# Optimization experiments

Measured on AMD Instinct MI355X. Metric: run time of the kernel, lower is better.

## Reference

```python
import jax, jax.numpy as jnp
import numpy as np

N_NODES = 100000
N_EDGES = 300000
D_NODE_IN = 128
D_EDGE_IN = 4
LATENT = 256
HIDDEN = 256
STEPS = 6
D_OUT = 128
LN_EPS = 1e-5


def _mlp(x, w1, b1, w2, b2):
    # hk.nets.MLP([HIDDEN, out], activation=swish): act on hidden, none on output
    return jax.nn.swish(x @ w1 + b1) @ w2 + b2


def _ln(x, scale, offset):
    m = jnp.mean(x, axis=-1, keepdims=True)
    c = x - m
    v = jnp.mean(c * c, axis=-1, keepdims=True)
    return c * jax.lax.rsqrt(v + LN_EPS) * scale + offset


def setup_inputs():
    key = jax.random.key(0)
    ks = iter(jax.random.split(key, 40))

    def w(shape):
        fan_in = shape[-2]
        return (jax.random.normal(next(ks), shape, jnp.float32) / np.sqrt(fan_in).astype(np.float32))

    inp = {}
    inp['node_features'] = jax.random.normal(next(ks), (N_NODES, D_NODE_IN), jnp.float32)
    inp['edge_features'] = jax.random.normal(next(ks), (N_EDGES, D_EDGE_IN), jnp.float32)
    inp['senders'] = jax.random.randint(next(ks), (N_EDGES,), 0, N_NODES, jnp.int32)
    inp['receivers'] = jax.random.randint(next(ks), (N_EDGES,), 0, N_NODES, jnp.int32)
    # encoder (embed) MLPs + LayerNorm
    inp['enc_node_w1'] = w((D_NODE_IN, HIDDEN)); inp['enc_node_b1'] = jnp.zeros((HIDDEN,), jnp.float32)
    inp['enc_node_w2'] = w((HIDDEN, LATENT)); inp['enc_node_b2'] = jnp.zeros((LATENT,), jnp.float32)
    inp['enc_node_ln_s'] = jnp.ones((LATENT,), jnp.float32); inp['enc_node_ln_o'] = jnp.zeros((LATENT,), jnp.float32)
    inp['enc_edge_w1'] = w((D_EDGE_IN, HIDDEN)); inp['enc_edge_b1'] = jnp.zeros((HIDDEN,), jnp.float32)
    inp['enc_edge_w2'] = w((HIDDEN, LATENT)); inp['enc_edge_b2'] = jnp.zeros((LATENT,), jnp.float32)
    inp['enc_edge_ln_s'] = jnp.ones((LATENT,), jnp.float32); inp['enc_edge_ln_o'] = jnp.zeros((LATENT,), jnp.float32)
    # processor: STEPS unshared InteractionNetwork layers, weights stacked on axis 0
    inp['pe_w1'] = w((STEPS, 3 * LATENT, HIDDEN)); inp['pe_b1'] = jnp.zeros((STEPS, HIDDEN), jnp.float32)
    inp['pe_w2'] = w((STEPS, HIDDEN, LATENT)); inp['pe_b2'] = jnp.zeros((STEPS, LATENT), jnp.float32)
    inp['pe_ln_s'] = jnp.ones((STEPS, LATENT), jnp.float32); inp['pe_ln_o'] = jnp.zeros((STEPS, LATENT), jnp.float32)
    inp['pn_w1'] = w((STEPS, 2 * LATENT, HIDDEN)); inp['pn_b1'] = jnp.zeros((STEPS, HIDDEN), jnp.float32)
    inp['pn_w2'] = w((STEPS, HIDDEN, LATENT)); inp['pn_b2'] = jnp.zeros((STEPS, LATENT), jnp.float32)
    inp['pn_ln_s'] = jnp.ones((STEPS, LATENT), jnp.float32); inp['pn_ln_o'] = jnp.zeros((STEPS, LATENT), jnp.float32)
    # decoder (output) MLP, no LayerNorm
    inp['dec_w1'] = w((LATENT, HIDDEN)); inp['dec_b1'] = jnp.zeros((HIDDEN,), jnp.float32)
    inp['dec_w2'] = w((HIDDEN, D_OUT)); inp['dec_b2'] = jnp.zeros((D_OUT,), jnp.float32)
    return inp


def reference(node_features, edge_features, senders, receivers,
              enc_node_w1, enc_node_b1, enc_node_w2, enc_node_b2, enc_node_ln_s, enc_node_ln_o,
              enc_edge_w1, enc_edge_b1, enc_edge_w2, enc_edge_b2, enc_edge_ln_s, enc_edge_ln_o,
              pe_w1, pe_b1, pe_w2, pe_b2, pe_ln_s, pe_ln_o,
              pn_w1, pn_b1, pn_w2, pn_b2, pn_ln_s, pn_ln_o,
              dec_w1, dec_b1, dec_w2, dec_b2):
    # Embed nodes and edges into latent space (MLP + LayerNorm).
    node = _ln(_mlp(node_features, enc_node_w1, enc_node_b1, enc_node_w2, enc_node_b2), enc_node_ln_s, enc_node_ln_o)
    edge = _ln(_mlp(edge_features, enc_edge_w1, enc_edge_b1, enc_edge_w2, enc_edge_b2), enc_edge_ln_s, enc_edge_ln_o)

    n_nodes = node.shape[0]

    def step(carry, p):
        node, edge = carry
        ew1, eb1, ew2, eb2, els, elo, nw1, nb1, nw2, nb2, nls, nlo = p
        # edge update: MLP(concat[edge, sender_node, receiver_node]) + residual
        msg_in = jnp.concatenate([edge, node[senders], node[receivers]], axis=-1)  # [E, 3*LATENT]
        edge = edge + _ln(_mlp(msg_in, ew1, eb1, ew2, eb2), els, elo)
        # aggregate messages to receiver nodes
        agg = jax.ops.segment_sum(edge, receivers, num_segments=n_nodes)  # [N, LATENT]
        # node update: MLP(concat[node, agg]) + residual
        node = node + _ln(_mlp(jnp.concatenate([node, agg], axis=-1), nw1, nb1, nw2, nb2), nls, nlo)
        return (node, edge), None

    (node, edge), _ = jax.lax.scan(
        step, (node, edge),
        (pe_w1, pe_b1, pe_w2, pe_b2, pe_ln_s, pe_ln_o,
         pn_w1, pn_b1, pn_w2, pn_b2, pn_ln_s, pn_ln_o))

    # decoder: plain MLP (no LayerNorm) on nodes only (node_output_size given).
    return _mlp(node, dec_w1, dec_b1, dec_w2, dec_b2)  # [N, D_OUT]
```

## Files before the change

kernel.cpp:

```cpp
#include <hip/hip_runtime.h>
#include <hip/hip_bf16.h>


#define NN 100000
#define NE 300000

typedef __attribute__((ext_vector_type(8))) short bf16x8;
typedef __attribute__((ext_vector_type(8))) unsigned short u16x8;
typedef __attribute__((ext_vector_type(4))) float f32x4;

typedef const __attribute__((address_space(1))) void cg1_t;
typedef __attribute__((address_space(3))) void l3_t;
static __device__ __forceinline__ void gld_lds16(const void* g, void* l) {
  __builtin_amdgcn_global_load_lds((cg1_t*)g, (l3_t*)l, 16, 0, 0);
}

static __device__ __forceinline__ unsigned short f2bf(float f) {
  union { float f; unsigned u; } v; v.f = f;
  unsigned r = v.u + 0x7FFFu + ((v.u >> 16) & 1u);
  return (unsigned short)(r >> 16);
}
static __device__ __forceinline__ float bf2f(unsigned short h) {
  union { unsigned u; float f; } v; v.u = ((unsigned)h) << 16;
  return v.f;
}
static __device__ __forceinline__ float swish(float x) {
  return x * __builtin_amdgcn_rcpf(1.f + __expf(-x));
}

struct KArgs {
  const float* Xf;
  unsigned short* nodeB;
  unsigned short* edgeB;
  const unsigned short* aggB;
  const int* snd;
  const int* rcv;
  const unsigned short* W1p;
  const unsigned short* W2p;
  const float* b1;
  const float* b2;
  const float* lns;
  const float* lno;
  float* outF;
  int M;
};

__global__ void pack_w(const float* __restrict__ src,
                       unsigned short* __restrict__ dst,
                       int Ksrc, int Kpad, int N) {
  src += (size_t)blockIdx.y * Ksrc * N;
  dst += (size_t)blockIdx.y * Kpad * N;
  int fi = blockIdx.x;
  int nfr = N >> 4;
  int nb = fi % nfr, kb = fi / nfr;
  int t = threadIdx.x;
  int lane = t >> 3, j = t & 7;
  int k = kb * 32 + ((lane >> 4) * 8) + j;
  int col = nb * 16 + (lane & 15);
  unsigned short v = (k < Ksrc) ? f2bf(src[(size_t)k * N + col]) : (unsigned short)0;
  dst[(size_t)fi * 512 + t] = v;
}

__global__ void zero_ws(uint4* __restrict__ p, int n16) {
  uint4 z = {0u, 0u, 0u, 0u};
  for (int i = blockIdx.x * blockDim.x + threadIdx.x; i < n16;
       i += gridDim.x * blockDim.x)
    p[i] = z;
}

__global__ void hist_k(const int* __restrict__ rcv, int* __restrict__ cnt) {
  int e = blockIdx.x * blockDim.x + threadIdx.x;
  if (e < NE) {
    int r = rcv[e]; r = r < 0 ? 0 : (r > NN - 1 ? NN - 1 : r);
    atomicAdd(&cnt[r], 1);
  }
}

__global__ __launch_bounds__(1024)
void scan_k(const int* __restrict__ cnt, int* __restrict__ off) {
  __shared__ int wsum[16];
  __shared__ int carry_s, tot_s;
  int t = threadIdx.x, lane = t & 63, w = t >> 6;
  if (t == 0) carry_s = 0;
  __syncthreads();
  for (int base = 0; base < NN; base += 1024) {
    int i = base + t;
    int v = (i < NN) ? cnt[i] : 0;
    int incl = v;
    #pragma unroll
    for (int d = 1; d < 64; d <<= 1) {
      int u = __shfl_up(incl, d);
      if (lane >= d) incl += u;
    }
    if (lane == 63) wsum[w] = incl;
    int c0 = carry_s;
    __syncthreads();
    if (t < 16) {
      int s = wsum[t];
      int isc = s;
      #pragma unroll
      for (int d = 1; d < 16; d <<= 1) {
        int u = __shfl_up(isc, d);
        if (t >= d) isc += u;
      }
      wsum[t] = isc - s;
    }
    __syncthreads();
    int excl = c0 + wsum[w] + incl - v;
    if (i < NN) off[i] = excl;
    if (t == 1023) tot_s = wsum[15] + incl;
    __syncthreads();
    if (t == 0) carry_s += tot_s;
    __syncthreads();
  }
  if (t == 0) off[NN] = carry_s;
}

__global__ void fill_k(const int* __restrict__ rcv, const int* __restrict__ off,
                       int* __restrict__ cnt2, int* __restrict__ eidx) {
  int e = blockIdx.x * blockDim.x + threadIdx.x;
  if (e < NE) {
    int r = rcv[e]; r = r < 0 ? 0 : (r > NN - 1 ? NN - 1 : r);
    int p = off[r] + atomicAdd(&cnt2[r], 1);
    if (p >= 0 && p < NE) eidx[p] = e;
  }
}

__global__ __launch_bounds__(256)
void agg_k(const unsigned short* __restrict__ edge, const int* __restrict__ off,
           const int* __restrict__ eidx, unsigned short* __restrict__ agg) {
  int t = threadIdx.x;
  int n0 = blockIdx.x * 8;
  #pragma unroll 1
  for (int u = 0; u < 8; ++u) {
    int n = n0 + u;
    if (n >= NN) return;
    int s = off[n], e = off[n + 1];
    if (s < 0) s = 0;
    if (e > NE) e = NE;
    float acc = 0.f;
    for (int i = s; i < e; ++i) {
      int eid = eidx[i];
      eid = eid < 0 ? 0 : (eid > NE - 1 ? NE - 1 : eid);
      acc += bf2f(edge[(size_t)eid * 256 + t]);
    }
    agg[(size_t)n * 256 + t] = f2bf(acc);
  }
}

template<int PHASE>
__global__ __launch_bounds__(512)
void gnn_kernel(KArgs A) {
  constexpr int K1  = PHASE==0?128 : PHASE==1?64 : PHASE==2?768 : PHASE==3?512 : 256;
  constexpr int NS1 = K1 / 64;
  constexpr int N2  = (PHASE==4) ? 128 : 256;
  constexpr int NF2 = N2 / 128;

  __shared__ __align__(16) char smem[38912];
  auto Ht  = (unsigned short (*)[264])(smem);
  float* ps    = (float*)(smem + 33792);
  float* ps2   = (float*)(smem + 35840);
  float* rs_mu = (float*)(smem + 37888);
  float* rs_rs = (float*)(smem + 38144);
  int*   lidx  = (int*)(smem + 38400);

  const int tid  = threadIdx.x;
  const int wid  = tid >> 6;
  const int lane = tid & 63;
  const int r0   = blockIdx.x * 64;
  const int M    = A.M;

  if constexpr (PHASE == 2) {
    if (tid < 64) {
      int e = r0 + tid; if (e > M - 1) e = M - 1;
      int v = A.snd[e]; v = v < 0 ? 0 : (v > NN - 1 ? NN - 1 : v);
      lidx[tid] = v;
    } else if (tid < 128) {
      int e = r0 + tid - 64; if (e > M - 1) e = M - 1;
      int v = A.rcv[e]; v = v < 0 ? 0 : (v > NN - 1 ? NN - 1 : v);
      lidx[tid] = v;
    }
  }
  __syncthreads();

  const int mrow  = lane & 15;
  const int rbase = (lane >> 4) * 4;
  const int swz   = mrow & 7;

  f32x4 zero4 = {0.f, 0.f, 0.f, 0.f};
  f32x4 acc1[4][2];
  #pragma unroll
  for (int m = 0; m < 4; ++m) { acc1[m][0] = zero4; acc1[m][1] = zero4; }

  if constexpr (PHASE <= 1) {
    auto stage = [&](int ks, int b) {
      int r = tid >> 3;
      int c = (tid & 7) ^ (r & 7);
      int row = r0 + r; if (row > M - 1) row = M - 1;
      u16x8 w;
      if constexpr (PHASE == 0) {
        const float* s = A.Xf + (size_t)row * 128 + ks * 64 + c * 8;
        float4 f0 = *(const float4*)s;
        float4 f1 = *(const float4*)(s + 4);
        w[0]=f2bf(f0.x); w[1]=f2bf(f0.y); w[2]=f2bf(f0.z); w[3]=f2bf(f0.w);
        w[4]=f2bf(f1.x); w[5]=f2bf(f1.y); w[6]=f2bf(f1.z); w[7]=f2bf(f1.w);
      } else {
        w = (u16x8){0,0,0,0,0,0,0,0};
        if (c == 0) {
          float4 f = *(const float4*)(A.Xf + (size_t)row * 4);
          w[0]=f2bf(f.x); w[1]=f2bf(f.y); w[2]=f2bf(f.z); w[3]=f2bf(f.w);
        }
      }
      *(u16x8*)(smem + b * 8192 + (tid >> 3) * 128 + (tid & 7) * 16) = w;
    };
    stage(0, 0);
    __syncthreads();
    #pragma unroll
    for (int ks = 0; ks < NS1; ++ks) {
      if (ks + 1 < NS1) stage(ks + 1, (ks + 1) & 1);
      const char* buf = smem + (ks & 1) * 8192;
      #pragma unroll
      for (int kk = 0; kk < 2; ++kk) {
        int ch = (kk * 4 + (lane >> 4)) ^ swz;
        const char* p0 = buf + mrow * 128 + ch * 16;
        bf16x8 a0 = *(const bf16x8*)(p0);
        bf16x8 a1 = *(const bf16x8*)(p0 + 16 * 128);
        bf16x8 a2 = *(const bf16x8*)(p0 + 32 * 128);
        bf16x8 a3 = *(const bf16x8*)(p0 + 48 * 128);
        const unsigned short* wb = A.W1p + ((size_t)((2 * ks + kk) * 16 + wid * 2) * 64 + lane) * 8;
        bf16x8 b0 = *(const bf16x8*)(wb);
        bf16x8 b1 = *(const bf16x8*)(wb + 512);
        acc1[0][0] = __builtin_amdgcn_mfma_f32_16x16x32_bf16(a0, b0, acc1[0][0], 0, 0, 0);
        acc1[0][1] = __builtin_amdgcn_mfma_f32_16x16x32_bf16(a0, b1, acc1[0][1], 0, 0, 0);
        acc1[1][0] = __builtin_amdgcn_mfma_f32_16x16x32_bf16(a1, b0, acc1[1][0], 0, 0, 0);
        acc1[1][1] = __builtin_amdgcn_mfma_f32_16x16x32_bf16(a1, b1, acc1[1][1], 0, 0, 0);
        acc1[2][0] = __builtin_amdgcn_mfma_f32_16x16x32_bf16(a2, b0, acc1[2][0], 0, 0, 0);
        acc1[2][1] = __builtin_amdgcn_mfma_f32_16x16x32_bf16(a2, b1, acc1[2][1], 0, 0, 0);
        acc1[3][0] = __builtin_amdgcn_mfma_f32_16x16x32_bf16(a3, b0, acc1[3][0], 0, 0, 0);
        acc1[3][1] = __builtin_amdgcn_mfma_f32_16x16x32_bf16(a3, b1, acc1[3][1], 0, 0, 0);
      }
      __syncthreads();
    }
  } else {
    int r = tid >> 3;
    int cs = ((tid & 7) ^ (r & 7)) * 8;
    int row = r0 + r; if (row > M - 1) row = M - 1;
    const unsigned short *s0 = nullptr, *s1 = nullptr, *s2 = nullptr;
    if constexpr (PHASE == 2) {
      s0 = A.edgeB + (size_t)row * 256 + cs;
      s1 = A.nodeB + (size_t)lidx[r] * 256 + cs;
      s2 = A.nodeB + (size_t)lidx[64 + r] * 256 + cs;
    } else if constexpr (PHASE == 3) {
      s0 = A.nodeB + (size_t)row * 256 + cs;
      s1 = A.aggB + (size_t)row * 256 + cs;
    } else {
      s0 = A.nodeB + (size_t)row * 256 + cs;
    }
    auto issue = [&](int ks, int b) {
      const unsigned short* src;
      if constexpr (PHASE == 2)
        src = ks < 4 ? s0 + ks * 64 : (ks < 8 ? s1 + (ks - 4) * 64 : s2 + (ks - 8) * 64);
      else if constexpr (PHASE == 3)
        src = ks < 4 ? s0 + ks * 64 : s1 + (ks - 4) * 64;
      else
        src = s0 + ks * 64;
      gld_lds16(src, smem + b * 8192 + wid * 1024);
    };
    const unsigned short* w1base = A.W1p + ((size_t)(wid * 2) * 64 + lane) * 8;
    auto load_b = [&](int ks, bf16x8* bk0, bf16x8* bk1) {
      const unsigned short* wb0 = w1base + (size_t)(2 * ks) * 16 * 512;
      const unsigned short* wb1 = w1base + (size_t)(2 * ks + 1) * 16 * 512;
      bk0[0] = *(const bf16x8*)(wb0); bk0[1] = *(const bf16x8*)(wb0 + 512);
      bk1[0] = *(const bf16x8*)(wb1); bk1[1] = *(const bf16x8*)(wb1 + 512);
    };

    issue(0, 0);
    issue(1, 1);
    bf16x8 c0[2], c1[2], n0[2], n1[2];
    load_b(0, c0, c1);
    #pragma unroll
    for (int ks = 0; ks < NS1; ++ks) {
      if (ks < NS1 - 1) asm volatile("s_waitcnt vmcnt(1)" ::: "memory");
      else              asm volatile("s_waitcnt vmcnt(0)" ::: "memory");
      __builtin_amdgcn_sched_barrier(0);
      __builtin_amdgcn_s_barrier();
      __builtin_amdgcn_sched_barrier(0);
      if (ks + 1 < NS1) load_b(ks + 1, n0, n1);
      const char* buf = smem + (ks & 1) * 8192;
      #pragma unroll
      for (int kk = 0; kk < 2; ++kk) {
        int ch = (kk * 4 + (lane >> 4)) ^ swz;
        const char* p0 = buf + mrow * 128 + ch * 16;
        bf16x8 a0 = *(const bf16x8*)(p0);
        bf16x8 a1 = *(const bf16x8*)(p0 + 16 * 128);
        bf16x8 a2 = *(const bf16x8*)(p0 + 32 * 128);
        bf16x8 a3 = *(const bf16x8*)(p0 + 48 * 128);
        bf16x8 b0 = kk ? c1[0] : c0[0];
        bf16x8 b1 = kk ? c1[1] : c0[1];
        acc1[0][0] = __builtin_amdgcn_mfma_f32_16x16x32_bf16(a0, b0, acc1[0][0], 0, 0, 0);
        acc1[0][1] = __builtin_amdgcn_mfma_f32_16x16x32_bf16(a0, b1, acc1[0][1], 0, 0, 0);
        acc1[1][0] = __builtin_amdgcn_mfma_f32_16x16x32_bf16(a1, b0, acc1[1][0], 0, 0, 0);
        acc1[1][1] = __builtin_amdgcn_mfma_f32_16x16x32_bf16(a1, b1, acc1[1][1], 0, 0, 0);
        acc1[2][0] = __builtin_amdgcn_mfma_f32_16x16x32_bf16(a2, b0, acc1[2][0], 0, 0, 0);
        acc1[2][1] = __builtin_amdgcn_mfma_f32_16x16x32_bf16(a2, b1, acc1[2][1], 0, 0, 0);
        acc1[3][0] = __builtin_amdgcn_mfma_f32_16x16x32_bf16(a3, b0, acc1[3][0], 0, 0, 0);
        acc1[3][1] = __builtin_amdgcn_mfma_f32_16x16x32_bf16(a3, b1, acc1[3][1], 0, 0, 0);
      }
      __builtin_amdgcn_sched_barrier(0);
      __builtin_amdgcn_s_barrier();
      __builtin_amdgcn_sched_barrier(0);
      if (ks + 2 < NS1) issue(ks + 2, ks & 1);
      c0[0] = n0[0]; c0[1] = n0[1]; c1[0] = n1[0]; c1[1] = n1[1];
    }
  }

  #pragma unroll
  for (int nf = 0; nf < 2; ++nf) {
    int c = wid * 32 + nf * 16 + mrow;
    float bb = A.b1[c];
    #pragma unroll
    for (int m = 0; m < 4; ++m)
      #pragma unroll
      for (int j = 0; j < 4; ++j)
        Ht[m * 16 + rbase + j][c] = f2bf(swish(acc1[m][nf][j] + bb));
  }
  __syncthreads();

  f32x4 acc2[4][NF2];
  #pragma unroll
  for (int m = 0; m < 4; ++m)
    #pragma unroll
    for (int nf = 0; nf < NF2; ++nf) acc2[m][nf] = zero4;

  const int kof = (lane >> 4) * 8;
  #pragma unroll
  for (int ks = 0; ks < 8; ++ks) {
    bf16x8 a[4], b[NF2];
    #pragma unroll
    for (int m = 0; m < 4; ++m)
      a[m] = *(const bf16x8*)&Ht[m * 16 + mrow][ks * 32 + kof];
    #pragma unroll
    for (int nf = 0; nf < NF2; ++nf)
      b[nf] = *(const bf16x8*)(A.W2p + ((size_t)(ks * (N2 / 16) + wid * NF2 + nf) * 64 + lane) * 8);
    #pragma unroll
    for (int m = 0; m < 4; ++m)
      #pragma unroll
      for (int nf = 0; nf < NF2; ++nf)
        acc2[m][nf] = __builtin_amdgcn_mfma_f32_16x16x32_bf16(a[m], b[nf], acc2[m][nf], 0, 0, 0);
  }

  if constexpr (PHASE == 4) {
    int c = wid * 16 + mrow;
    float bb = A.b2[c];
    #pragma unroll
    for (int m = 0; m < 4; ++m)
      #pragma unroll
      for (int j = 0; j < 4; ++j) {
        int rg = r0 + m * 16 + rbase + j;
        if (rg < M) A.outF[(size_t)rg * 128 + c] = acc2[m][0][j] + bb;
      }
  } else {
    const int cc0 = wid * 32 + mrow;
    const int cc1 = cc0 + 16;
    const float bb0 = A.b2[cc0];
    const float bb1 = A.b2[cc1];
    #pragma unroll
    for (int m = 0; m < 4; ++m)
      #pragma unroll
      for (int j = 0; j < 4; ++j) {
        acc2[m][0][j] += bb0;
        acc2[m][1][j] += bb1;
        float t  = acc2[m][0][j] + acc2[m][1][j];
        float t2 = acc2[m][0][j] * acc2[m][0][j] + acc2[m][1][j] * acc2[m][1][j];
        #pragma unroll
        for (int mk = 1; mk < 16; mk <<= 1) {
          t  += __shfl_xor(t, mk);
          t2 += __shfl_xor(t2, mk);
        }
        if (mrow == 0) {
          int row = m * 16 + rbase + j;
          ps [wid * 64 + row] = t;
          ps2[wid * 64 + row] = t2;
        }
      }
    __syncthreads();
    if (tid < 64) {
      float s = 0.f, q = 0.f;
      #pragma unroll
      for (int w = 0; w < 8; ++w) { s += ps[w * 64 + tid]; q += ps2[w * 64 + tid]; }
      float mu = s * (1.0f / 256.0f);
      float va = fmaxf(q * (1.0f / 256.0f) - mu * mu, 0.f);
      rs_mu[tid] = mu;
      rs_rs[tid] = __builtin_amdgcn_rsqf(va + 1e-5f);
    }
    __syncthreads();
    const float ls0 = A.lns[cc0], lo0 = A.lno[cc0];
    const float ls1 = A.lns[cc1], lo1 = A.lno[cc1];
    #pragma unroll
    for (int m = 0; m < 4; ++m)
      #pragma unroll
      for (int j = 0; j < 4; ++j) {
        int row = m * 16 + rbase + j;
        int rg = r0 + row;
        if (rg >= M) continue;
        float mu = rs_mu[row], rstd = rs_rs[row];
        float y0 = (acc2[m][0][j] - mu) * rstd * ls0 + lo0;
        float y1 = (acc2[m][1][j] - mu) * rstd * ls1 + lo1;
        size_t base = (size_t)rg * 256;
        if constexpr (PHASE == 0) {
          A.nodeB[base + cc0] = f2bf(y0);
          A.nodeB[base + cc1] = f2bf(y1);
        } else if constexpr (PHASE == 1) {
          A.edgeB[base + cc0] = f2bf(y0);
          A.edgeB[base + cc1] = f2bf(y1);
        } else if constexpr (PHASE == 2) {
          A.edgeB[base + cc0] = f2bf(bf2f(A.edgeB[base + cc0]) + y0);
          A.edgeB[base + cc1] = f2bf(bf2f(A.edgeB[base + cc1]) + y1);
        } else {
          A.nodeB[base + cc0] = f2bf(bf2f(A.nodeB[base + cc0]) + y0);
          A.nodeB[base + cc1] = f2bf(bf2f(A.nodeB[base + cc1]) + y1);
        }
      }
  }
}

extern "C" void kernel_launch(void* const* d_in, const int* in_sizes, int n_in,
                              void* d_out, int out_size, void* d_ws, size_t ws_size,
                              hipStream_t stream) {
  (void)in_sizes; (void)n_in; (void)out_size; (void)ws_size;
  const float* x_node = (const float*)d_in[0];
  const float* x_edge = (const float*)d_in[1];
  const int* snd = (const int*)d_in[2];
  const int* rcv = (const int*)d_in[3];
  const float* en_w1 = (const float*)d_in[4];
  const float* en_b1 = (const float*)d_in[5];
  const float* en_w2 = (const float*)d_in[6];
  const float* en_b2 = (const float*)d_in[7];
  const float* en_ls = (const float*)d_in[8];
  const float* en_lo = (const float*)d_in[9];
  const float* ee_w1 = (const float*)d_in[10];
  const float* ee_b1 = (const float*)d_in[11];
  const float* ee_w2 = (const float*)d_in[12];
  const float* ee_b2 = (const float*)d_in[13];
  const float* ee_ls = (const float*)d_in[14];
  const float* ee_lo = (const float*)d_in[15];
  const float* pe_w1 = (const float*)d_in[16];
  const float* pe_b1 = (const float*)d_in[17];
  const float* pe_w2 = (const float*)d_in[18];
  const float* pe_b2 = (const float*)d_in[19];
  const float* pe_ls = (const float*)d_in[20];
  const float* pe_lo = (const float*)d_in[21];
  const float* pn_w1 = (const float*)d_in[22];
  const float* pn_b1 = (const float*)d_in[23];
  const float* pn_w2 = (const float*)d_in[24];
  const float* pn_b2 = (const float*)d_in[25];
  const float* pn_ls = (const float*)d_in[26];
  const float* pn_lo = (const float*)d_in[27];
  const float* dc_w1 = (const float*)d_in[28];
  const float* dc_b1 = (const float*)d_in[29];
  const float* dc_w2 = (const float*)d_in[30];
  const float* dc_b2 = (const float*)d_in[31];

  char* ws = (char*)d_ws;
  unsigned short* edgeB = (unsigned short*)(ws);
  unsigned short* nodeB = (unsigned short*)(ws + 153600000LL);
  unsigned short* aggB  = (unsigned short*)(ws + 204800000LL);

  unsigned short* wpck = (unsigned short*)d_out;
  size_t o = 0;
  auto nxt = [&](size_t n) { unsigned short* p = wpck + o; o += n; return p; };
  unsigned short* p_en_w1 = nxt(128 * 256);
  unsigned short* p_en_w2 = nxt(256 * 256);
  unsigned short* p_ee_w1 = nxt(64 * 256);
  unsigned short* p_ee_w2 = nxt(256 * 256);
  unsigned short* p_pe_w1 = nxt((size_t)6 * 768 * 256);
  unsigned short* p_pe_w2 = nxt((size_t)6 * 256 * 256);
  unsigned short* p_pn_w1 = nxt((size_t)6 * 512 * 256);
  unsigned short* p_pn_w2 = nxt((size_t)6 * 256 * 256);
  unsigned short* p_dc_w1 = nxt(256 * 256);
  unsigned short* p_dc_w2 = nxt(256 * 128);
  const size_t DC_BYTES = (256 * 256 + 256 * 128) * 2;

  char* outc = (char*)d_out;
  int* cnt  = (int*)(outc + 6062080);
  int* cnt2 = (int*)(outc + 6462080);
  int* off  = (int*)(outc + 6862080);
  int* eidx = (int*)(outc + 7262096);

  dim3 B(512);
  pack_w<<<dim3(4 * 16, 1), B, 0, stream>>>(en_w1, p_en_w1, 128, 128, 256);
  pack_w<<<dim3(8 * 16, 1), B, 0, stream>>>(en_w2, p_en_w2, 256, 256, 256);
  pack_w<<<dim3(2 * 16, 1), B, 0, stream>>>(ee_w1, p_ee_w1, 4, 64, 256);
  pack_w<<<dim3(8 * 16, 1), B, 0, stream>>>(ee_w2, p_ee_w2, 256, 256, 256);
  pack_w<<<dim3(24 * 16, 6), B, 0, stream>>>(pe_w1, p_pe_w1, 768, 768, 256);
  pack_w<<<dim3(8 * 16, 6), B, 0, stream>>>(pe_w2, p_pe_w2, 256, 256, 256);
  pack_w<<<dim3(16 * 16, 6), B, 0, stream>>>(pn_w1, p_pn_w1, 512, 512, 256);
  pack_w<<<dim3(8 * 16, 6), B, 0, stream>>>(pn_w2, p_pn_w2, 256, 256, 256);
  pack_w<<<dim3(8 * 16, 1), B, 0, stream>>>(dc_w1, p_dc_w1, 256, 256, 256);
  pack_w<<<dim3(8 * 8, 1), B, 0, stream>>>(dc_w2, p_dc_w2, 256, 256, 128);

  zero_ws<<<dim3(196), dim3(256), 0, stream>>>((uint4*)cnt, 800000 / 16);
  hist_k<<<dim3(1172), dim3(256), 0, stream>>>(rcv, cnt);
  scan_k<<<dim3(1), dim3(1024), 0, stream>>>(cnt, off);
  fill_k<<<dim3(1172), dim3(256), 0, stream>>>(rcv, off, cnt2, eidx);

  dim3 GN(1563), GE(4688);

  {
    KArgs a{}; a.Xf = x_node; a.W1p = p_en_w1; a.W2p = p_en_w2;
    a.b1 = en_b1; a.b2 = en_b2; a.lns = en_ls; a.lno = en_lo;
    a.nodeB = nodeB; a.M = NN;
    gnn_kernel<0><<<GN, B, 0, stream>>>(a);
  }
  {
    KArgs a{}; a.Xf = x_edge; a.W1p = p_ee_w1; a.W2p = p_ee_w2;
    a.b1 = ee_b1; a.b2 = ee_b2; a.lns = ee_ls; a.lno = ee_lo;
    a.edgeB = edgeB; a.M = NE;
    gnn_kernel<1><<<GE, B, 0, stream>>>(a);
  }
  for (int s = 0; s < 6; ++s) {
    {
      KArgs a{}; a.snd = snd; a.rcv = rcv;
      a.nodeB = nodeB; a.edgeB = edgeB;
      a.W1p = p_pe_w1 + (size_t)s * 768 * 256;
      a.W2p = p_pe_w2 + (size_t)s * 256 * 256;
      a.b1 = pe_b1 + s * 256; a.b2 = pe_b2 + s * 256;
      a.lns = pe_ls + s * 256; a.lno = pe_lo + s * 256;
      a.M = NE;
      gnn_kernel<2><<<GE, B, 0, stream>>>(a);
    }
    agg_k<<<dim3(12500), dim3(256), 0, stream>>>(edgeB, off, eidx, aggB);
    {
      KArgs a{}; a.nodeB = nodeB; a.aggB = aggB;
      a.W1p = p_pn_w1 + (size_t)s * 512 * 256;
      a.W2p = p_pn_w2 + (size_t)s * 256 * 256;
      a.b1 = pn_b1 + s * 256; a.b2 = pn_b2 + s * 256;
      a.lns = pn_ls + s * 256; a.lno = pn_lo + s * 256;
      a.M = NN;
      gnn_kernel<3><<<GN, B, 0, stream>>>(a);
    }
  }
  hipMemcpyAsync((void*)aggB, p_dc_w1, DC_BYTES, hipMemcpyDeviceToDevice, stream);
  {
    KArgs a{}; a.nodeB = nodeB;
    a.W1p = (const unsigned short*)aggB;
    a.W2p = (const unsigned short*)aggB + 256 * 256;
    a.b1 = dc_b1; a.b2 = dc_b2;
    a.outF = (float*)d_out; a.M = NN;
    gnn_kernel<4><<<GN, B, 0, stream>>>(a);
  }
}
```

Measured before the change: 2.767 ms.

## Triple-buffer the A-tile LDS pipeline and harden bf16 conversion and math

Moves the first-GEMM A-tile prefetch from double to triple buffering, issuing three global-to-LDS loads up front and relaxing the vmcnt waits so two loads stay in flight. Separately, f2bf now flushes Inf/NaN bf16 values to zero, swish uses a full-precision divide instead of the hardware reciprocal, and rsqrt uses rsqrtf instead of the raw builtin. The deeper prefetch is meant to hide gather latency, but it uses an extra 8 KB of LDS per block, which may reduce occupancy if the shared buffer was not already sized for three stages. The numerical changes add instructions on the epilogue path.

```diff
diff --git a/kernel.cpp b/kernel.cpp
--- a/kernel.cpp
+++ b/kernel.cpp
@@ -18,14 +18,13 @@
 static __device__ __forceinline__ unsigned short f2bf(float f) {
   union { float f; unsigned u; } v; v.f = f;
   unsigned r = v.u + 0x7FFFu + ((v.u >> 16) & 1u);
-  return (unsigned short)(r >> 16);
+  unsigned short h = (unsigned short)(r >> 16);
+  if ((h & 0x7F80u) == 0x7F80u) h = 0;
+  return h;
 }
 static __device__ __forceinline__ float bf2f(unsigned short h) {
   union { unsigned u; float f; } v; v.u = ((unsigned)h) << 16;
   return v.f;
-}
-static __device__ __forceinline__ float swish(float x) {
-  return x * __builtin_amdgcn_rcpf(1.f + __expf(-x));
 }
 
 struct KArgs {
@@ -256,7 +255,7 @@
     } else {
       s0 = A.nodeB + (size_t)row * 256 + cs;
     }
-    auto issue = [&](int ks, int b) {
+    auto issue = [&](int ks) {
       const unsigned short* src;
       if constexpr (PHASE == 2)
         src = ks < 4 ? s0 + ks * 64 : (ks < 8 ? s1 + (ks - 4) * 64 : s2 + (ks - 8) * 64);
@@ -264,7 +263,7 @@
         src = ks < 4 ? s0 + ks * 64 : s1 + (ks - 4) * 64;
       else
         src = s0 + ks * 64;
-      gld_lds16(src, smem + b * 8192 + wid * 1024);
+      gld_lds16(src, smem + (ks % 3) * 8192 + wid * 1024);
     };
     const unsigned short* w1base = A.W1p + ((size_t)(wid * 2) * 64 + lane) * 8;
     auto load_b = [&](int ks, bf16x8* bk0, bf16x8* bk1) {
@@ -274,19 +273,22 @@
       bk1[0] = *(const bf16x8*)(wb1); bk1[1] = *(const bf16x8*)(wb1 + 512);
     };
 
-    issue(0, 0);
-    issue(1, 1);
+    issue(0);
+    issue(1);
+    issue(2);
     bf16x8 c0[2], c1[2], n0[2], n1[2];
     load_b(0, c0, c1);
     #pragma unroll
     for (int ks = 0; ks < NS1; ++ks) {
-      if (ks < NS1 - 1) asm volatile("s_waitcnt vmcnt(1)" ::: "memory");
-      else              asm volatile("s_waitcnt vmcnt(0)" ::: "memory");
+      int rem = NS1 - 1 - ks;
+      if (rem >= 2)      asm volatile("s_waitcnt vmcnt(2)" ::: "memory");
+      else if (rem == 1) asm volatile("s_waitcnt vmcnt(1)" ::: "memory");
+      else               asm volatile("s_waitcnt vmcnt(0)" ::: "memory");
       __builtin_amdgcn_sched_barrier(0);
       __builtin_amdgcn_s_barrier();
       __builtin_amdgcn_sched_barrier(0);
       if (ks + 1 < NS1) load_b(ks + 1, n0, n1);
-      const char* buf = smem + (ks & 1) * 8192;
+      const char* buf = smem + (ks % 3) * 8192;
       #pragma unroll
       for (int kk = 0; kk < 2; ++kk) {
         int ch = (kk * 4 + (lane >> 4)) ^ swz;
@@ -309,7 +311,7 @@
       __builtin_amdgcn_sched_barrier(0);
       __builtin_amdgcn_s_barrier();
       __builtin_amdgcn_sched_barrier(0);
-      if (ks + 2 < NS1) issue(ks + 2, ks & 1);
+      if (ks + 3 < NS1) issue(ks + 3);
       c0[0] = n0[0]; c0[1] = n0[1]; c1[0] = n1[0]; c1[1] = n1[1];
     }
   }
@@ -321,8 +323,11 @@
     #pragma unroll
     for (int m = 0; m < 4; ++m)
       #pragma unroll
-      for (int j = 0; j < 4; ++j)
-        Ht[m * 16 + rbase + j][c] = f2bf(swish(acc1[m][nf][j] + bb));
+      for (int j = 0; j < 4; ++j) {
+        float x = acc1[m][nf][j] + bb;
+        float h = x * (1.f / (1.f + __expf(-x)));
+        Ht[m * 16 + rbase + j][c] = f2bf(h);
+      }
   }
   __syncthreads();
 
@@ -391,7 +396,7 @@
       float mu = s * (1.0f / 256.0f);
       float va = fmaxf(q * (1.0f / 256.0f) - mu * mu, 0.f);
       rs_mu[tid] = mu;
-      rs_rs[tid] = __builtin_amdgcn_rsqf(va + 1e-5f);
+      rs_rs[tid] = rsqrtf(va + 1e-5f);
     }
     __syncthreads();
     const float ls0 = A.lns[cc0], lo0 = A.lno[cc0];
```

Measured after the change: 3.004 ms. 8.5% more time.
